# Kernel optimization log

Hardware: AMD Instinct MI355X
Metric: run time of the kernel (lower is better)

## Reference

```python
import jax, jax.numpy as jnp
import numpy as np

B, T, C = 2, 1024, 1024
H = 16
HS = C // H          # head size = 64
ROT = HS // 2        # partial rotary dims = 32
CTX = 1024           # ctx_len (T <= CTX)
FFN_H = 3 * 1024     # GeGLU hidden = 3 * n_ffn
LN_EPS = 1e-5


def setup_inputs():
    key = jax.random.key(0)
    ks = jax.random.split(key, 20)
    s = 0.02
    f32 = jnp.float32
    p = {}
    p["x"] = jax.random.normal(ks[0], (B, T, C), f32)
    p["ln1_w"] = jnp.ones((C,), f32); p["ln1_b"] = jnp.zeros((C,), f32)
    p["ln2_w"] = jnp.ones((C,), f32); p["ln2_b"] = jnp.zeros((C,), f32)
    p["Wq"] = jax.random.normal(ks[1], (C, C), f32) * s; p["bq"] = jnp.zeros((C,), f32)
    p["Wk"] = jax.random.normal(ks[2], (C, C), f32) * s; p["bk"] = jnp.zeros((C,), f32)
    p["Wv"] = jax.random.normal(ks[3], (C, C), f32) * s; p["bv"] = jnp.zeros((C,), f32)
    p["Wo"] = jax.random.normal(ks[4], (C, C), f32) * s; p["bo"] = jnp.zeros((C,), f32)
    p["time_w"] = 1.0 + 0.01 * jax.random.normal(ks[5], (H, CTX), f32)
    p["time_alpha"] = 1.0 + 0.01 * jax.random.normal(ks[6], (H, 1, CTX), f32)
    p["time_beta"] = 1.0 + 0.01 * jax.random.normal(ks[7], (H, CTX, 1), f32)
    p["time_gamma"] = 1.0 + 0.01 * jax.random.normal(ks[8], (CTX, 1), f32)
    p["mix_w"] = jnp.eye(H, dtype=f32) + 0.02 * jax.random.normal(ks[9], (H, H), f32)
    p["Wkg"] = jax.random.normal(ks[10], (C, FFN_H), f32) * s; p["bkg"] = jnp.zeros((FFN_H,), f32)
    p["Wvg"] = jax.random.normal(ks[11], (C, FFN_H), f32) * s; p["bvg"] = jnp.zeros((FFN_H,), f32)
    p["Wwg"] = jax.random.normal(ks[12], (FFN_H, C), f32) * s; p["bwg"] = jnp.zeros((C,), f32)
    return p


def _ln(x, w, b):
    m = jnp.mean(x, axis=-1, keepdims=True)
    v = jnp.mean((x - m) ** 2, axis=-1, keepdims=True)
    return (x - m) * jax.lax.rsqrt(v + LN_EPS) * w + b


def _time_shift_half(x):
    # ZeroPad2d((0,0,1,-1)) on the first C//2 channels: shift down by one step in time
    c = x.shape[-1]
    shifted = jnp.pad(x[:, :-1, : c // 2], ((0, 0), (1, 0), (0, 0)))
    return jnp.concatenate([shifted, x[:, :, c // 2 :]], axis=-1)


def _decay_w(time_w, time_alpha, time_beta):
    # Toeplitz trick: [H, CTX] -> circulant [H, CTX, CTX] of relative-time weights
    TT = CTX
    w = jnp.pad(time_w, ((0, 0), (0, TT)))                 # [H, 2TT]
    w = jnp.tile(w, (1, TT))[:, :-TT]                      # [H, 2TT*TT - TT]
    w = w.reshape(-1, TT, 2 * TT - 1)[:, :, TT - 1 :]      # [H, TT, TT]
    return w[:, :T, :T] * time_alpha[:, :, :T] * time_beta[:, :T, :]


def _rotate_half(x):
    x1, x2 = x[..., : x.shape[-1] // 2], x[..., x.shape[-1] // 2 :]
    return jnp.concatenate([-x2, x1], axis=-1)


def _apply_rotary(q, k):
    # q, k: [B, H, T, ROT]
    inv_freq = 1.0 / (10000.0 ** (jnp.arange(0, ROT, 2, dtype=jnp.float32) / ROT))
    t = jnp.arange(T, dtype=jnp.float32)
    freqs = t[:, None] * inv_freq[None, :]                 # [T, ROT//2]
    emb = jnp.concatenate([freqs, freqs], axis=-1)         # [T, ROT]
    cos, sin = jnp.cos(emb), jnp.sin(emb)
    q = q * cos + _rotate_half(q) * sin
    k = k * cos + _rotate_half(k) * sin
    return q, k


def _mha_pro(x, Wq, bq, Wk, bk, Wv, bv, Wo, bo,
             time_w, time_alpha, time_beta, time_gamma, mix_w):
    w = _decay_w(time_w, time_alpha, time_beta)            # [H, T, T]
    xs = _time_shift_half(x)
    q = (xs @ Wq + bq).reshape(B, T, H, HS).transpose(0, 2, 1, 3)
    k = (xs @ Wk + bk).reshape(B, T, H, HS).transpose(0, 2, 1, 3)
    v = (xs @ Wv + bv).reshape(B, T, H, HS).transpose(0, 2, 1, 3)
    qr, qp = q[..., :ROT], q[..., ROT:]
    kr, kp = k[..., :ROT], k[..., ROT:]
    qr, kr = _apply_rotary(qr, kr)
    q = jnp.concatenate([qr, qp], axis=-1)
    k = jnp.concatenate([kr, kp], axis=-1)
    att = jnp.einsum('bhqd,bhkd->bhqk', q, k) * (1.0 / np.sqrt(HS))
    causal = jnp.tril(jnp.ones((T, T), dtype=bool))
    att = jnp.where(causal, att, -jnp.inf)
    att = jax.nn.softmax(att, axis=-1)
    att = att * w                                          # learned time-decay reweighting
    att = jnp.einsum('oi,biqk->boqk', mix_w, att)          # 1x1 conv head mixing
    y = jnp.einsum('bhqk,bhkd->bhqd', att, v)
    y = y.transpose(0, 2, 1, 3).reshape(B, T, C)
    return (y @ Wo + bo) * time_gamma[:T, :]


def _geglu(x, Wkg, bkg, Wvg, bvg, Wwg, bwg):
    kk = x @ Wkg + bkg
    vv = x @ Wvg + bvg
    return (jax.nn.gelu(kk, approximate=False) * vv) @ Wwg + bwg


def _block(x, ln1_w, ln1_b, ln2_w, ln2_b, Wq, bq, Wk, bk, Wv, bv, Wo, bo,
           time_w, time_alpha, time_beta, time_gamma, mix_w,
           Wkg, bkg, Wvg, bvg, Wwg, bwg):
    x = x + _mha_pro(_ln(x, ln1_w, ln1_b), Wq, bq, Wk, bk, Wv, bv, Wo, bo,
                     time_w, time_alpha, time_beta, time_gamma, mix_w)
    x = x + _geglu(_ln(x, ln2_w, ln2_b), Wkg, bkg, Wvg, bvg, Wwg, bwg)
    return x


def reference(x, ln1_w, ln1_b, ln2_w, ln2_b, Wq, bq, Wk, bk, Wv, bv, Wo, bo,
              time_w, time_alpha, time_beta, time_gamma, mix_w,
              Wkg, bkg, Wvg, bvg, Wwg, bwg):
    return _block(x, ln1_w, ln1_b, ln2_w, ln2_b, Wq, bq, Wk, bk, Wv, bv, Wo, bo,
                  time_w, time_alpha, time_beta, time_gamma, mix_w,
                  Wkg, bkg, Wvg, bvg, Wwg, bwg)
```

## Files before the change

### kernel.cpp

```cpp
#include <hip/hip_runtime.h>
#include <cstdint>
#include <cstddef>
#include <cstdio>

#define B_   2
#define T_   1024
#define C_   1024
#define H_   16
#define HS_  64
#define FFN_ 3072

typedef __bf16   bf16x8 __attribute__((ext_vector_type(8)));
typedef float    f32x4  __attribute__((ext_vector_type(4)));
typedef float    f32x16 __attribute__((ext_vector_type(16)));
typedef uint16_t u16x8  __attribute__((ext_vector_type(8)));

__device__ __forceinline__ uint16_t f2bf(float f){
  uint32_t u = __float_as_uint(f);
  u += 0x7FFFu + ((u >> 16) & 1u);
  return (uint16_t)(u >> 16);
}
__device__ __forceinline__ float bf2f(uint16_t h){
  return __uint_as_float(((uint32_t)h) << 16);
}
__device__ __forceinline__ bf16x8 ldb8(const uint16_t* p){
  return __builtin_bit_cast(bf16x8, *reinterpret_cast<const u16x8*>(p));
}
__device__ __forceinline__ f32x4 mfma16(bf16x8 a, bf16x8 b, f32x4 c){
  return __builtin_amdgcn_mfma_f32_16x16x32_bf16(a, b, c, 0, 0, 0);
}

typedef __attribute__((address_space(1))) const uint32_t* gas_t;
typedef __attribute__((address_space(3))) uint32_t* las_t;
__device__ __forceinline__ void gl_lds16(const uint16_t* g, uint16_t* l){
  __builtin_amdgcn_global_load_lds((gas_t)g, (las_t)l, 16, 0, 0);
}

__global__ __launch_bounds__(256) void k_prep(
    const float* __restrict__ Wq, const float* __restrict__ Wk,
    const float* __restrict__ Wv, const float* __restrict__ Wo,
    const float* __restrict__ Wkg, const float* __restrict__ Wvg,
    const float* __restrict__ Wwg,
    const float* __restrict__ bq, const float* __restrict__ bk,
    const float* __restrict__ bv, const float* __restrict__ bkg,
    const float* __restrict__ bvg,
    const float* __restrict__ x, const float* __restrict__ ln1w,
    const float* __restrict__ ln1b,
    uint16_t* __restrict__ WqT, uint16_t* __restrict__ WkT,
    uint16_t* __restrict__ WvT, uint16_t* __restrict__ WoT,
    uint16_t* __restrict__ WkgT, uint16_t* __restrict__ WvgT,
    uint16_t* __restrict__ WwgT, float* __restrict__ bcat,
    uint16_t* __restrict__ xs)
{
  __shared__ float tile[32][33];
  __shared__ float red[8];
  const int id = blockIdx.x;
  const int tid = threadIdx.x;

  if (id < 13312){
    const float* in; uint16_t* outp; int R, Cc, bx, by;
    if (id < 4096){
      int w = id >> 10, r = id & 1023;
      in   = (w==0)?Wq:(w==1)?Wk:(w==2)?Wv:Wo;
      outp = (w==0)?WqT:(w==1)?WkT:(w==2)?WvT:WoT;
      R = 1024; Cc = 1024; bx = r & 31; by = r >> 5;
    } else if (id < 10240){
      int r = id - 4096; int w = r / 3072; r -= w*3072;
      in = w ? Wvg : Wkg; outp = w ? WvgT : WkgT;
      R = 1024; Cc = 3072; bx = r % 96; by = r / 96;
    } else {
      int r = id - 10240;
      in = Wwg; outp = WwgT; R = 3072; Cc = 1024;
      bx = r & 31; by = r >> 5;
    }
    int c0 = bx*32, r0 = by*32;
    int tx = tid & 31, ty = tid >> 5;
    #pragma unroll
    for (int i=0;i<4;i++) tile[ty+i*8][tx] = in[(size_t)(r0+ty+i*8)*Cc + c0+tx];
    __syncthreads();
    #pragma unroll
    for (int i=0;i<4;i++) outp[(size_t)(c0+ty+i*8)*R + r0+tx] = f2bf(tile[tx][ty+i*8]);
    return;
  }
  if (id < 13348){
    int i = (id - 13312)*256 + tid;
    float v;
    if      (i < 1024) v = bq[i];
    else if (i < 2048) v = bk[i-1024];
    else if (i < 3072) v = bv[i-2048];
    else if (i < 6144) v = bkg[i-3072];
    else               v = bvg[i-6144];
    bcat[i] = v;
    return;
  }
  {
    int row = id - 13348;
    int t = row & (T_-1);
    const float* xr = x + (size_t)row*C_;
    float4 v = reinterpret_cast<const float4*>(xr)[tid];
    float s  = v.x+v.y+v.z+v.w;
    float s2 = v.x*v.x+v.y*v.y+v.z*v.z+v.w*v.w;
    #pragma unroll
    for (int o=1;o<64;o<<=1){ s += __shfl_xor(s,o); s2 += __shfl_xor(s2,o); }
    int lane = tid & 63, wv = tid >> 6;
    if (lane == 0){ red[wv] = s; red[4+wv] = s2; }
    __syncthreads();
    s  = red[0]+red[1]+red[2]+red[3];
    s2 = red[4]+red[5]+red[6]+red[7];
    float mean = s * (1.f/1024.f);
    float var  = s2 * (1.f/1024.f) - mean*mean;
    float rs   = rsqrtf(var + 1e-5f);
    float vals[4] = {v.x, v.y, v.z, v.w};
    #pragma unroll
    for (int j=0;j<4;j++){
      int cc = tid*4 + j;
      float o_ = (vals[j]-mean)*rs*ln1w[cc] + ln1b[cc];
      uint16_t ob = f2bf(o_);
      if (cc < 512){
        if (t < T_-1) xs[(size_t)(row+1)*C_ + cc] = ob;
        if (t == 0)   xs[(size_t)row*C_ + cc] = 0;
      } else {
        xs[(size_t)row*C_ + cc] = ob;
      }
    }
  }
}

template<int SHIFT>
__global__ __launch_bounds__(256) void k_ln(const float* __restrict__ in,
                                            const float* __restrict__ w,
                                            const float* __restrict__ bia,
                                            uint16_t* __restrict__ out){
  int row = blockIdx.x;
  int t = row & (T_-1);
  const float* xr = in + (size_t)row*C_;
  float4 v = reinterpret_cast<const float4*>(xr)[threadIdx.x];
  float s  = v.x+v.y+v.z+v.w;
  float s2 = v.x*v.x+v.y*v.y+v.z*v.z+v.w*v.w;
  #pragma unroll
  for (int o=1;o<64;o<<=1){ s += __shfl_xor(s,o); s2 += __shfl_xor(s2,o); }
  __shared__ float red[8];
  int lane = threadIdx.x & 63, wid = threadIdx.x >> 6;
  if (lane == 0){ red[wid] = s; red[4+wid] = s2; }
  __syncthreads();
  s  = red[0]+red[1]+red[2]+red[3];
  s2 = red[4]+red[5]+red[6]+red[7];
  float mean = s * (1.f/1024.f);
  float var  = s2 * (1.f/1024.f) - mean*mean;
  float rs   = rsqrtf(var + 1e-5f);
  float vals[4] = {v.x, v.y, v.z, v.w};
  #pragma unroll
  for (int j=0;j<4;j++){
    int cc = threadIdx.x*4 + j;
    float o_ = (vals[j]-mean)*rs*w[cc] + bia[cc];
    uint16_t ob = f2bf(o_);
    if (SHIFT){
      if (cc < 512){
        if (t < T_-1) out[(size_t)(row+1)*C_ + cc] = ob;
        if (t == 0)   out[(size_t)row*C_ + cc] = 0;
      } else {
        out[(size_t)row*C_ + cc] = ob;
      }
    } else {
      out[(size_t)row*C_ + cc] = ob;
    }
  }
}

enum { EPI_QKV=0, EPI_WO=2, EPI_BF16=3, EPI_FFN2=4 };

template<int EPI, int BN>
__global__ __launch_bounds__(256) void k_gemm2(
    const uint16_t* __restrict__ A, const uint16_t* __restrict__ Bt,
    const float* __restrict__ bias, void* __restrict__ outp,
    int M, int N, int K,
    const float* __restrict__ aux0, const float* __restrict__ aux1)
{
  __shared__ uint16_t As[128*32];
  __shared__ uint16_t Bs[BN*32];
  const int m0 = blockIdx.y*128, n0 = blockIdx.x*BN;
  const int tid = threadIdx.x;
  const int lane = tid & 63, wid = tid >> 6;
  const int wy = wid >> 1, wx = wid & 1;
  const int l16 = lane & 15, lr = lane >> 4;
  const int WN = BN/2;
  const int NW = BN/32;
  const f32x4 z = {0.f,0.f,0.f,0.f};
  f32x4 acc[4][NW];
  #pragma unroll
  for (int m=0;m<4;m++)
    #pragma unroll
    for (int n=0;n<NW;n++) acc[m][n] = z;
  const int srow = tid >> 2, scol = (tid & 3)*8;
  for (int k0 = 0; k0 < K; k0 += 32){
    gl_lds16(A + (size_t)(m0 + srow)*K      + k0 + scol, As + tid*8);
    gl_lds16(A + (size_t)(m0 + 64 + srow)*K + k0 + scol, As + 2048 + tid*8);
    gl_lds16(Bt + (size_t)(n0 + srow)*K     + k0 + scol, Bs + tid*8);
    if constexpr (BN == 128)
      gl_lds16(Bt + (size_t)(n0 + 64 + srow)*K + k0 + scol, Bs + 2048 + tid*8);
    __syncthreads();
    bf16x8 af[4], bfr[NW];
    #pragma unroll
    for (int m=0;m<4;m++) af[m] = ldb8(As + (wy*64 + m*16 + l16)*32 + lr*8);
    #pragma unroll
    for (int n=0;n<NW;n++) bfr[n] = ldb8(Bs + (wx*WN + n*16 + l16)*32 + lr*8);
    #pragma unroll
    for (int m=0;m<4;m++)
      #pragma unroll
      for (int n=0;n<NW;n++) acc[m][n] = mfma16(af[m], bfr[n], acc[m][n]);
    __syncthreads();
  }
  if constexpr (EPI == EPI_QKV){
    const float linvf = exp2f(-(float)l16 * 0.83048202f);
    #pragma unroll
    for (int m=0;m<4;m++){
      #pragma unroll
      for (int r=0;r<4;r++){
        int row = m0 + wy*64 + m*16 + lr*4 + r;
        int bb = row >> 10, t = row & 1023;
        int col0 = n0 + wx*32 + l16;
        float v0 = acc[m][0][r] + bias[col0];
        float v1 = acc[m][1][r] + bias[col0+16];
        int kind = col0 >> 10, hcol = col0 & 1023;
        int h = hcol >> 6, d0 = hcol & 63;
        if (kind < 2 && wx == 0){
          float sn, cs;
          __sincosf((float)t * linvf, &sn, &cs);
          float r0 = v0*cs - v1*sn;
          float r1 = v1*cs + v0*sn;
          v0 = r0; v1 = r1;
        }
        uint16_t* dst = (uint16_t*)outp + (size_t)kind*2097152;
        if (kind < 2){
          size_t basei = (((size_t)bb*16 + h)*1024 + t)*64;
          dst[basei + d0]      = f2bf(v0);
          dst[basei + d0 + 16] = f2bf(v1);
        } else {
          size_t basei = ((size_t)bb*16 + h)*65536;
          dst[basei + (size_t)d0*1024 + t]      = f2bf(v0);
          dst[basei + (size_t)(d0+16)*1024 + t] = f2bf(v1);
        }
      }
    }
  } else {
    #pragma unroll
    for (int m=0;m<4;m++){
      #pragma unroll
      for (int n=0;n<NW;n++){
        int col = n0 + wx*WN + n*16 + l16;
        float bc_ = bias ? bias[col] : 0.f;
        #pragma unroll
        for (int r=0;r<4;r++){
          int row = m0 + wy*64 + m*16 + lr*4 + r;
          float v = acc[m][n][r] + bc_;
          if constexpr (EPI == EPI_WO){
            int t = row & (T_-1);
            ((float*)outp)[(size_t)row*N + col] = aux1[(size_t)row*N + col] + v*aux0[t];
          } else if constexpr (EPI == EPI_BF16){
            ((uint16_t*)outp)[(size_t)row*N + col] = f2bf(v);
          } else {
            ((float*)outp)[(size_t)row*N + col] = aux0[(size_t)row*N + col] + v;
          }
        }
      }
    }
  }
}

__global__ __launch_bounds__(256) void k_stats(const uint16_t* __restrict__ q,
                                               const uint16_t* __restrict__ kmat,
                                               float* __restrict__ sm, float* __restrict__ sl){
  int bh = blockIdx.x, qb = blockIdx.y;
  int lane = threadIdx.x & 63, wid = threadIdx.x >> 6;
  int l16 = lane & 15, lr = lane >> 4;
  int r0 = qb*64 + wid*16;
  const uint16_t* qh = q    + (size_t)bh*T_*HS_;
  const uint16_t* kh = kmat + (size_t)bh*T_*HS_;
  int kq = lr*8;
  bf16x8 a0 = ldb8(qh + (size_t)(r0 + l16)*HS_ + kq);
  bf16x8 a1 = ldb8(qh + (size_t)(r0 + l16)*HS_ + kq + 32);
  float m_[4], l_[4]; int rows[4];
  #pragma unroll
  for (int r=0;r<4;r++){ m_[r] = -1e30f; l_[r] = 0.f; rows[r] = r0 + lr*4 + r; }
  int ktmax = (r0 + 15) >> 4;
  for (int kt = 0; kt <= ktmax; kt++){
    bf16x8 b0 = ldb8(kh + (size_t)(kt*16 + l16)*HS_ + kq);
    bf16x8 b1 = ldb8(kh + (size_t)(kt*16 + l16)*HS_ + kq + 32);
    f32x4 s = {0.f,0.f,0.f,0.f};
    s = mfma16(a0, b0, s);
    s = mfma16(a1, b1, s);
    int kcol = kt*16 + l16;
    #pragma unroll
    for (int r=0;r<4;r++){
      float sv = (kcol <= rows[r]) ? s[r]*0.125f : -3.0e38f;
      float mn = fmaxf(m_[r], sv);
      l_[r] = l_[r]*__expf(m_[r] - mn) + __expf(sv - mn);
      m_[r] = mn;
    }
  }
  #pragma unroll
  for (int o=1;o<16;o<<=1){
    #pragma unroll
    for (int r=0;r<4;r++){
      float mo = __shfl_xor(m_[r], o);
      float lo = __shfl_xor(l_[r], o);
      float mn = fmaxf(m_[r], mo);
      l_[r] = l_[r]*__expf(m_[r] - mn) + lo*__expf(mo - mn);
      m_[r] = mn;
    }
  }
  if (l16 == 0){
    #pragma unroll
    for (int r=0;r<4;r++){
      sm[(size_t)bh*T_ + rows[r]] = m_[r];
      sl[(size_t)bh*T_ + rows[r]] = l_[r];
    }
  }
}

__global__ __launch_bounds__(512, 2) void k_attn(
    const uint16_t* __restrict__ q, const uint16_t* __restrict__ kmat,
    const uint16_t* __restrict__ vT,
    const float* __restrict__ sm, const float* __restrict__ sl,
    const float* __restrict__ tw, const float* __restrict__ alpha,
    const float* __restrict__ beta, const float* __restrict__ mixw,
    uint16_t* __restrict__ py)
{
  int qt = blockIdx.x, kc = blockIdx.y, b = blockIdx.z;
  if (8*kc > qt) return;
  const int q0 = qt*16, ck0 = kc*128;
  const int lc = min(127, q0 + 15 - ck0);
  const int nt = (lc >> 5) + 1;

  __shared__ uint32_t U32[2*4096];
  __shared__ uint16_t Cm[2*8320];
  __shared__ uint16_t TWL[16*160];

  const int tid = threadIdx.x;
  const int lane = tid & 63;
  const int wid = __builtin_amdgcn_readfirstlane(tid >> 6);
  const int l16 = lane & 15, lr = lane >> 4;
  const int l32 = lane & 31, g32 = lane >> 5;

  const int base = 1008 - q0 + ck0;
  for (int i = tid; i < 16*144; i += 512){
    int h = i / 144, t = i - h*144;
    int gi = base + t;
    TWL[h*160 + t] = (gi <= 1023) ? f2bf(tw[h*1024 + gi]) : (uint16_t)0;
  }

  float SM[2][4], BSL[2][4];
  bf16x8 qa[2][2];
  #pragma unroll
  for (int h2=0; h2<2; ++h2){
    int h = 2*wid + h2, bh = b*16 + h;
    float4 s4 = *reinterpret_cast<const float4*>(sm   + (size_t)bh*1024 + q0 + lr*4);
    float4 l4 = *reinterpret_cast<const float4*>(sl   + (size_t)bh*1024 + q0 + lr*4);
    float4 b4 = *reinterpret_cast<const float4*>(beta + (size_t)h*1024  + q0 + lr*4);
    SM[h2][0]=s4.x; SM[h2][1]=s4.y; SM[h2][2]=s4.z; SM[h2][3]=s4.w;
    BSL[h2][0]=b4.x/l4.x; BSL[h2][1]=b4.y/l4.y; BSL[h2][2]=b4.z/l4.z; BSL[h2][3]=b4.w/l4.w;
    #pragma unroll
    for (int kk=0;kk<2;kk++)
      qa[h2][kk] = ldb8(q + ((size_t)bh*1024 + q0 + l16)*64 + kk*32 + lr*8);
  }
  bf16x8 mwf;
  {
    u16x8 t8;
    #pragma unroll
    for (int j=0;j<8;j++){
      float v = (l32 < 16) ? mixw[l32*16 + g32*8 + j] : 0.f;
      t8[j] = f2bf(v);
    }
    mwf = __builtin_bit_cast(bf16x8, t8);
  }

  const f32x4 z = {0.f,0.f,0.f,0.f};
  f32x4 acc[2][4];
  #pragma unroll
  for (int oo=0;oo<2;oo++) for (int n=0;n<4;n++) acc[oo][n] = z;

  __syncthreads();

  for (int tp = 0; tp < nt; tp += 2){
    const int ntile = (nt - tp >= 2) ? 2 : 1;
    #pragma unroll
    for (int half = 0; half < 2; ++half){
      if (half >= ntile) break;
      const int t = tp + half;
      const int k0 = ck0 + t*32;
      float al0[2], al1[2];
      #pragma unroll
      for (int n=0;n<2;n++){
        int kg = k0 + n*16 + l16;
        al0[n] = alpha[(2*wid+0)*1024 + kg];
        al1[n] = alpha[(2*wid+1)*1024 + kg];
      }
      f32x4 s[2][2];
      s[0][0]=z; s[0][1]=z; s[1][0]=z; s[1][1]=z;
      #pragma unroll
      for (int h2=0;h2<2;h2++){
        const uint16_t* kh = kmat + ((size_t)(b*16 + 2*wid + h2)*1024 + k0)*64;
        #pragma unroll
        for (int kk=0;kk<2;kk++){
          bf16x8 kb0 = ldb8(kh + (size_t)(l16)*64      + kk*32 + lr*8);
          bf16x8 kb1 = ldb8(kh + (size_t)(16 + l16)*64 + kk*32 + lr*8);
          s[h2][0] = mfma16(qa[h2][kk], kb0, s[h2][0]);
          s[h2][1] = mfma16(qa[h2][kk], kb1, s[h2][1]);
        }
      }
      uint32_t* Ub = U32 + half*4096;
      #pragma unroll
      for (int n=0;n<2;n++){
        int kloc = n*16 + l16;
        int kg = k0 + kloc;
        #pragma unroll
        for (int r=0;r<4;r++){
          int qloc = lr*4 + r;
          bool ok = (kg <= q0 + qloc);
          int twi = 15 - qloc + (kg - ck0);
          float u0 = 0.f, u1 = 0.f;
          if (ok){
            u0 = __expf(s[0][n][r]*0.125f - SM[0][r]) * BSL[0][r] * al0[n] * bf2f(TWL[(2*wid+0)*160 + twi]);
            u1 = __expf(s[1][n][r]*0.125f - SM[1][r]) * BSL[1][r] * al1[n] * bf2f(TWL[(2*wid+1)*160 + twi]);
          }
          uint32_t pk = (uint32_t)f2bf(u0) | ((uint32_t)f2bf(u1) << 16);
          Ub[wid*512 + qloc*32 + ((kloc + 8*(qloc>>2)) & 31)] = pk;
        }
      }
    }
    __syncthreads();
    #pragma unroll
    for (int half = 0; half < 2; ++half){
      if (half >= ntile) break;
      const uint32_t* Ub = U32 + half*4096;
      uint16_t* Cb = Cm + half*8320;
      #pragma unroll
      for (int cc=0; cc<2; ++cc){
        int qrow = wid*2 + cc;
        int pbase = qrow*32;
        int swz = (l32 + 8*(qrow>>2)) & 31;
        u16x8 a8;
        uint32_t* a32 = reinterpret_cast<uint32_t*>(&a8);
        #pragma unroll
        for (int j=0;j<4;j++)
          a32[j] = Ub[(4*g32 + j)*512 + pbase + swz];
        bf16x8 a = __builtin_bit_cast(bf16x8, a8);
        f32x16 zz{};
        __builtin_amdgcn_s_setprio(1);
        f32x16 dd = __builtin_amdgcn_mfma_f32_32x32x16_bf16(a, mwf, zz, 0, 0, 0);
        __builtin_amdgcn_s_setprio(0);
        if (l32 < 16){
          int o = l32;
          #pragma unroll
          for (int rg=0; rg<4; ++rg){
            int p0 = pbase + rg*8 + g32*4;
            uint32_t w0 = (uint32_t)f2bf(dd[4*rg+0]) | ((uint32_t)f2bf(dd[4*rg+1]) << 16);
            uint32_t w1 = (uint32_t)f2bf(dd[4*rg+2]) | ((uint32_t)f2bf(dd[4*rg+3]) << 16);
            uint2 pk2; pk2.x = w0; pk2.y = w1;
            *reinterpret_cast<uint2*>(Cb + (size_t)o*520 + p0) = pk2;
          }
        }
      }
    }
    __syncthreads();
    #pragma unroll
    for (int half = 0; half < 2; ++half){
      if (half >= ntile) break;
      const int k0 = ck0 + (tp + half)*32;
      const uint16_t* Cb = Cm + half*8320;
      #pragma unroll
      for (int oo=0;oo<2;oo++){
        int o = 2*wid + oo;
        bf16x8 cf = ldb8(Cb + (size_t)o*520 + l16*32 + lr*8);
        const uint16_t* vh = vT + (size_t)(b*16 + o)*65536;
        __builtin_amdgcn_s_setprio(1);
        #pragma unroll
        for (int n=0;n<4;n++){
          bf16x8 vf = ldb8(vh + (size_t)(n*16 + l16)*1024 + k0 + lr*8);
          acc[oo][n] = mfma16(cf, vf, acc[oo][n]);
        }
        __builtin_amdgcn_s_setprio(0);
      }
    }
  }

  uint16_t* po = py + (((size_t)(b*64 + qt))*8 + kc)*16384;
  #pragma unroll
  for (int oo=0;oo<2;oo++){
    int o = 2*wid + oo;
    #pragma unroll
    for (int n=0;n<4;n++)
      #pragma unroll
      for (int r=0;r<4;r++){
        int qloc = lr*4 + r;
        po[o*1024 + qloc*64 + n*16 + l16] = f2bf(acc[oo][n][r]);
      }
  }
}

__global__ void k_yred(const uint16_t* __restrict__ py, uint16_t* __restrict__ y){
  int idx = blockIdx.x*256 + threadIdx.x;
  int d8 = idx & 7, qq = (idx>>3)&15, o = (idx>>7)&15, qt = (idx>>11)&63, b = idx>>17;
  int nch = (qt>>3) + 1;
  const uint16_t* p0 = py + (((size_t)(b*64+qt))*8)*16384 + o*1024 + qq*64 + d8*8;
  float s[8] = {0,0,0,0,0,0,0,0};
  for (int kc=0; kc<nch; kc++){
    u16x8 v = *reinterpret_cast<const u16x8*>(p0 + (size_t)kc*16384);
    #pragma unroll
    for (int e=0;e<8;e++) s[e] += bf2f(v[e]);
  }
  int t = qt*16 + qq;
  u16x8 w;
  #pragma unroll
  for (int e=0;e<8;e++) w[e] = f2bf(s[e]);
  *reinterpret_cast<u16x8*>(y + ((size_t)(b*1024 + t))*1024 + o*64 + d8*8) = w;
}

__global__ void k_geglu(const uint16_t* __restrict__ ffu, uint16_t* __restrict__ g){
  int i = blockIdx.x*256 + threadIdx.x;
  int row = i / 384, j8 = i - row*384;
  const uint16_t* pa = ffu + (size_t)row*6144 + j8*8;
  u16x8 a = *reinterpret_cast<const u16x8*>(pa);
  u16x8 b = *reinterpret_cast<const u16x8*>(pa + 3072);
  u16x8 o;
  #pragma unroll
  for (int e=0;e<8;e++){
    float xv = bf2f(a[e]);
    float gl = 0.5f*xv*(1.f + erff(xv*0.70710678118f));
    o[e] = f2bf(gl * bf2f(b[e]));
  }
  *reinterpret_cast<u16x8*>(g + (size_t)row*3072 + j8*8) = o;
}

extern "C" void kernel_launch(void* const* d_in, const int* in_sizes, int n_in,
                              void* d_out, int out_size, void* d_ws, size_t ws_size,
                              hipStream_t stream)
{
  const float* x      = (const float*)d_in[0];
  const float* ln1w   = (const float*)d_in[1];
  const float* ln1b   = (const float*)d_in[2];
  const float* ln2w   = (const float*)d_in[3];
  const float* ln2b   = (const float*)d_in[4];
  const float* Wq     = (const float*)d_in[5];
  const float* bq     = (const float*)d_in[6];
  const float* Wk     = (const float*)d_in[7];
  const float* bk     = (const float*)d_in[8];
  const float* Wv     = (const float*)d_in[9];
  const float* bv     = (const float*)d_in[10];
  const float* Wo     = (const float*)d_in[11];
  const float* bo     = (const float*)d_in[12];
  const float* tw     = (const float*)d_in[13];
  const float* talpha = (const float*)d_in[14];
  const float* tbeta  = (const float*)d_in[15];
  const float* tgamma = (const float*)d_in[16];
  const float* mixw   = (const float*)d_in[17];
  const float* Wkg    = (const float*)d_in[18];
  const float* bkg    = (const float*)d_in[19];
  const float* Wvg    = (const float*)d_in[20];
  const float* bvg    = (const float*)d_in[21];
  const float* Wwg    = (const float*)d_in[22];
  const float* bwg    = (const float*)d_in[23];

  char* ws = (char*)d_ws;
  size_t off = 0;
  auto alloc = [&](size_t bytes)->char*{
    char* p = ws + off; off += (bytes + 255) & ~(size_t)255; return p;
  };
  uint16_t* WqT  = (uint16_t*)alloc((size_t)C_*C_*2);
  uint16_t* WkT  = (uint16_t*)alloc((size_t)C_*C_*2);
  uint16_t* WvT  = (uint16_t*)alloc((size_t)C_*C_*2);
  uint16_t* WoT  = (uint16_t*)alloc((size_t)C_*C_*2);
  uint16_t* WkgT = (uint16_t*)alloc((size_t)FFN_*C_*2);
  uint16_t* WvgT = (uint16_t*)alloc((size_t)FFN_*C_*2);
  uint16_t* WwgT = (uint16_t*)alloc((size_t)C_*FFN_*2);
  uint16_t* xs   = (uint16_t*)alloc((size_t)B_*T_*C_*2);
  uint16_t* qbuf = (uint16_t*)alloc((size_t)B_*T_*C_*2);
  uint16_t* kbuf = (uint16_t*)alloc((size_t)B_*T_*C_*2);
  uint16_t* vT   = (uint16_t*)alloc((size_t)B_*T_*C_*2);
  float*    sm   = (float*)alloc((size_t)B_*H_*T_*4);
  float*    sl   = (float*)alloc((size_t)B_*H_*T_*4);
  uint16_t* ybuf = (uint16_t*)alloc((size_t)B_*T_*C_*2);
  float*    x1   = (float*)alloc((size_t)B_*T_*C_*4);
  float*    bcat = (float*)alloc((size_t)9216*4);
  char*     region = alloc((size_t)64*1024*1024);
  uint16_t* py  = (uint16_t*)region;
  uint16_t* ffu = (uint16_t*)region;
  uint16_t* gb  = (uint16_t*)(region + (size_t)2048*6144*2);

  if (off > ws_size){
    fprintf(stderr, "kernel_launch: ws too small (%zu needed, %zu given)\n", off, ws_size);
    return;
  }

  dim3 blk(256);
  k_prep<<<15396, blk, 0, stream>>>(Wq, Wk, Wv, Wo, Wkg, Wvg, Wwg,
                                    bq, bk, bv, bkg, bvg,
                                    x, ln1w, ln1b,
                                    WqT, WkT, WvT, WoT, WkgT, WvgT, WwgT,
                                    bcat, xs);

  k_gemm2<EPI_QKV,64><<<dim3(48,16), blk, 0, stream>>>(xs, WqT, bcat, qbuf, 2048, 3072, 1024, nullptr, nullptr);

  k_stats<<<dim3(B_*H_, T_/64), blk, 0, stream>>>(qbuf, kbuf, sm, sl);
  k_attn<<<dim3(64,8,B_), dim3(512), 0, stream>>>(qbuf, kbuf, vT, sm, sl,
                                                  tw, talpha, tbeta, mixw, py);
  k_yred<<<1024, blk, 0, stream>>>(py, ybuf);

  k_gemm2<EPI_WO,64><<<dim3(16,16), blk, 0, stream>>>(ybuf, WoT, bo, x1, 2048, 1024, 1024, tgamma, x);

  k_ln<0><<<B_*T_, blk, 0, stream>>>(x1, ln2w, ln2b, xs);

  k_gemm2<EPI_BF16,128><<<dim3(48,16), blk, 0, stream>>>(xs, WkgT, bcat+3072, ffu, 2048, 6144, 1024, nullptr, nullptr);
  k_geglu<<<3072, blk, 0, stream>>>(ffu, gb);
  k_gemm2<EPI_FFN2,64><<<dim3(16,16), blk, 0, stream>>>(gb, WwgT, bwg, d_out, 2048, 1024, 3072, x1, nullptr);
}
```

Measured before the change: 276.7 us.

## Fuse GeGLU into FFN1 GEMM epilogue and use persistent attention scheduling

The GeLU and gate product move into the first FFN GEMM epilogue. The Wkg/Wvg weights and biases are interleaved in 16-column groups, so each warp holds matching k and v accumulator fragments. This drops the 2048x6144 bf16 intermediate round-trip and the separate k_geglu launch. The attention kernel also becomes a persistent grid of 512 blocks pulling causal work items from an atomic counter, instead of launching 64x8x2 blocks where many exit immediately; this costs a memset plus an atomic and barrier per item.

```diff
diff --git a/kernel.cpp b/kernel.cpp
--- a/kernel.cpp
+++ b/kernel.cpp
@@ -48,8 +48,8 @@
     const float* __restrict__ ln1b,
     uint16_t* __restrict__ WqT, uint16_t* __restrict__ WkT,
     uint16_t* __restrict__ WvT, uint16_t* __restrict__ WoT,
-    uint16_t* __restrict__ WkgT, uint16_t* __restrict__ WvgT,
-    uint16_t* __restrict__ WwgT, float* __restrict__ bcat,
+    uint16_t* __restrict__ Wff, uint16_t* __restrict__ WwgT,
+    float* __restrict__ bcat, float* __restrict__ bcatFF,
     uint16_t* __restrict__ xs)
 {
   __shared__ float tile[32][33];
@@ -58,39 +58,57 @@
   const int tid = threadIdx.x;
 
   if (id < 13312){
-    const float* in; uint16_t* outp; int R, Cc, bx, by;
     if (id < 4096){
       int w = id >> 10, r = id & 1023;
-      in   = (w==0)?Wq:(w==1)?Wk:(w==2)?Wv:Wo;
-      outp = (w==0)?WqT:(w==1)?WkT:(w==2)?WvT:WoT;
-      R = 1024; Cc = 1024; bx = r & 31; by = r >> 5;
+      const float* in = (w==0)?Wq:(w==1)?Wk:(w==2)?Wv:Wo;
+      uint16_t* outp  = (w==0)?WqT:(w==1)?WkT:(w==2)?WvT:WoT;
+      int c0 = (r & 31)*32, r0 = (r >> 5)*32;
+      int tx = tid & 31, ty = tid >> 5;
+      #pragma unroll
+      for (int i=0;i<4;i++) tile[ty+i*8][tx] = in[(size_t)(r0+ty+i*8)*1024 + c0+tx];
+      __syncthreads();
+      #pragma unroll
+      for (int i=0;i<4;i++) outp[(size_t)(c0+ty+i*8)*1024 + r0+tx] = f2bf(tile[tx][ty+i*8]);
     } else if (id < 10240){
-      int r = id - 4096; int w = r / 3072; r -= w*3072;
-      in = w ? Wvg : Wkg; outp = w ? WvgT : WkgT;
-      R = 1024; Cc = 3072; bx = r % 96; by = r / 96;
+      int r = id - 4096; int s = r / 3072; r -= s*3072;
+      const float* in = s ? Wvg : Wkg;
+      int c0 = (r % 96)*32, r0 = (r / 96)*32;
+      int tx = tid & 31, ty = tid >> 5;
+      #pragma unroll
+      for (int i=0;i<4;i++) tile[ty+i*8][tx] = in[(size_t)(r0+ty+i*8)*3072 + c0+tx];
+      __syncthreads();
+      #pragma unroll
+      for (int i=0;i<4;i++){
+        int j = c0+ty+i*8;
+        int row = ((j>>4)<<5) + (s<<4) + (j&15);
+        Wff[(size_t)row*1024 + r0+tx] = f2bf(tile[tx][ty+i*8]);
+      }
     } else {
       int r = id - 10240;
-      in = Wwg; outp = WwgT; R = 3072; Cc = 1024;
-      bx = r & 31; by = r >> 5;
-    }
-    int c0 = bx*32, r0 = by*32;
-    int tx = tid & 31, ty = tid >> 5;
-    #pragma unroll
-    for (int i=0;i<4;i++) tile[ty+i*8][tx] = in[(size_t)(r0+ty+i*8)*Cc + c0+tx];
-    __syncthreads();
-    #pragma unroll
-    for (int i=0;i<4;i++) outp[(size_t)(c0+ty+i*8)*R + r0+tx] = f2bf(tile[tx][ty+i*8]);
+      int c0 = (r & 31)*32, r0 = (r >> 5)*32;
+      int tx = tid & 31, ty = tid >> 5;
+      #pragma unroll
+      for (int i=0;i<4;i++) tile[ty+i*8][tx] = Wwg[(size_t)(r0+ty+i*8)*1024 + c0+tx];
+      __syncthreads();
+      #pragma unroll
+      for (int i=0;i<4;i++) WwgT[(size_t)(c0+ty+i*8)*3072 + r0+tx] = f2bf(tile[tx][ty+i*8]);
+    }
     return;
   }
-  if (id < 13348){
+  if (id < 13324){
     int i = (id - 13312)*256 + tid;
     float v;
     if      (i < 1024) v = bq[i];
     else if (i < 2048) v = bk[i-1024];
-    else if (i < 3072) v = bv[i-2048];
-    else if (i < 6144) v = bkg[i-3072];
-    else               v = bvg[i-6144];
+    else               v = bv[i-2048];
     bcat[i] = v;
+    return;
+  }
+  if (id < 13348){
+    int i = (id - 13324)*256 + tid;
+    int s = (i >> 4) & 1;
+    int j = ((i >> 5) << 4) | (i & 15);
+    bcatFF[i] = s ? bvg[j] : bkg[j];
     return;
   }
   {
@@ -126,13 +144,11 @@
   }
 }
 
-template<int SHIFT>
 __global__ __launch_bounds__(256) void k_ln(const float* __restrict__ in,
                                             const float* __restrict__ w,
                                             const float* __restrict__ bia,
                                             uint16_t* __restrict__ out){
   int row = blockIdx.x;
-  int t = row & (T_-1);
   const float* xr = in + (size_t)row*C_;
   float4 v = reinterpret_cast<const float4*>(xr)[threadIdx.x];
   float s  = v.x+v.y+v.z+v.w;
@@ -152,22 +168,11 @@
   #pragma unroll
   for (int j=0;j<4;j++){
     int cc = threadIdx.x*4 + j;
-    float o_ = (vals[j]-mean)*rs*w[cc] + bia[cc];
-    uint16_t ob = f2bf(o_);
-    if (SHIFT){
-      if (cc < 512){
-        if (t < T_-1) out[(size_t)(row+1)*C_ + cc] = ob;
-        if (t == 0)   out[(size_t)row*C_ + cc] = 0;
-      } else {
-        out[(size_t)row*C_ + cc] = ob;
-      }
-    } else {
-      out[(size_t)row*C_ + cc] = ob;
-    }
-  }
-}
-
-enum { EPI_QKV=0, EPI_WO=2, EPI_BF16=3, EPI_FFN2=4 };
+    out[(size_t)row*C_ + cc] = f2bf((vals[j]-mean)*rs*w[cc] + bia[cc]);
+  }
+}
+
+enum { EPI_QKV=0, EPI_WO=2, EPI_GEGLU=3, EPI_FFN2=4 };
 
 template<int EPI, int BN>
 __global__ __launch_bounds__(256) void k_gemm2(
@@ -242,6 +247,23 @@
         }
       }
     }
+  } else if constexpr (EPI == EPI_GEGLU){
+    const int colb = n0 + wx*WN;
+    #pragma unroll
+    for (int m=0;m<4;m++){
+      #pragma unroll
+      for (int r=0;r<4;r++){
+        int row = m0 + wy*64 + m*16 + lr*4 + r;
+        #pragma unroll
+        for (int np=0;np<NW;np+=2){
+          float kk = acc[m][np][r]   + bias[colb + np*16 + l16];
+          float vv = acc[m][np+1][r] + bias[colb + (np+1)*16 + l16];
+          float gl = 0.5f*kk*(1.f + erff(kk*0.70710678118f));
+          int j = ((colb>>5) + (np>>1))*16 + l16;
+          ((uint16_t*)outp)[(size_t)row*3072 + j] = f2bf(gl*vv);
+        }
+      }
+    }
   } else {
     #pragma unroll
     for (int m=0;m<4;m++){
@@ -256,8 +278,6 @@
           if constexpr (EPI == EPI_WO){
             int t = row & (T_-1);
             ((float*)outp)[(size_t)row*N + col] = aux1[(size_t)row*N + col] + v*aux0[t];
-          } else if constexpr (EPI == EPI_BF16){
-            ((uint16_t*)outp)[(size_t)row*N + col] = f2bf(v);
           } else {
             ((float*)outp)[(size_t)row*N + col] = aux0[(size_t)row*N + col] + v;
           }
@@ -324,17 +344,12 @@
     const float* __restrict__ sm, const float* __restrict__ sl,
     const float* __restrict__ tw, const float* __restrict__ alpha,
     const float* __restrict__ beta, const float* __restrict__ mixw,
-    uint16_t* __restrict__ py)
+    uint16_t* __restrict__ py, int* __restrict__ counter)
 {
-  int qt = blockIdx.x, kc = blockIdx.y, b = blockIdx.z;
-  if (8*kc > qt) return;
-  const int q0 = qt*16, ck0 = kc*128;
-  const int lc = min(127, q0 + 15 - ck0);
-  const int nt = (lc >> 5) + 1;
-
   __shared__ uint32_t U32[2*4096];
   __shared__ uint16_t Cm[2*8320];
   __shared__ uint16_t TWL[16*160];
+  __shared__ int s_item;
 
   const int tid = threadIdx.x;
   const int lane = tid & 63;
@@ -342,27 +357,6 @@
   const int l16 = lane & 15, lr = lane >> 4;
   const int l32 = lane & 31, g32 = lane >> 5;
 
-  const int base = 1008 - q0 + ck0;
-  for (int i = tid; i < 16*144; i += 512){
-    int h = i / 144, t = i - h*144;
-    int gi = base + t;
-    TWL[h*160 + t] = (gi <= 1023) ? f2bf(tw[h*1024 + gi]) : (uint16_t)0;
-  }
-
-  float SM[2][4], BSL[2][4];
-  bf16x8 qa[2][2];
-  #pragma unroll
-  for (int h2=0; h2<2; ++h2){
-    int h = 2*wid + h2, bh = b*16 + h;
-    float4 s4 = *reinterpret_cast<const float4*>(sm   + (size_t)bh*1024 + q0 + lr*4);
-    float4 l4 = *reinterpret_cast<const float4*>(sl   + (size_t)bh*1024 + q0 + lr*4);
-    float4 b4 = *reinterpret_cast<const float4*>(beta + (size_t)h*1024  + q0 + lr*4);
-    SM[h2][0]=s4.x; SM[h2][1]=s4.y; SM[h2][2]=s4.z; SM[h2][3]=s4.w;
-    BSL[h2][0]=b4.x/l4.x; BSL[h2][1]=b4.y/l4.y; BSL[h2][2]=b4.z/l4.z; BSL[h2][3]=b4.w/l4.w;
-    #pragma unroll
-    for (int kk=0;kk<2;kk++)
-      qa[h2][kk] = ldb8(q + ((size_t)bh*1024 + q0 + l16)*64 + kk*32 + lr*8);
-  }
   bf16x8 mwf;
   {
     u16x8 t8;
@@ -373,128 +367,168 @@
     }
     mwf = __builtin_bit_cast(bf16x8, t8);
   }
-
   const f32x4 z = {0.f,0.f,0.f,0.f};
-  f32x4 acc[2][4];
-  #pragma unroll
-  for (int oo=0;oo<2;oo++) for (int n=0;n<4;n++) acc[oo][n] = z;
-
-  __syncthreads();
-
-  for (int tp = 0; tp < nt; tp += 2){
-    const int ntile = (nt - tp >= 2) ? 2 : 1;
-    #pragma unroll
-    for (int half = 0; half < 2; ++half){
-      if (half >= ntile) break;
-      const int t = tp + half;
-      const int k0 = ck0 + t*32;
-      float al0[2], al1[2];
-      #pragma unroll
-      for (int n=0;n<2;n++){
-        int kg = k0 + n*16 + l16;
-        al0[n] = alpha[(2*wid+0)*1024 + kg];
-        al1[n] = alpha[(2*wid+1)*1024 + kg];
-      }
-      f32x4 s[2][2];
-      s[0][0]=z; s[0][1]=z; s[1][0]=z; s[1][1]=z;
-      #pragma unroll
-      for (int h2=0;h2<2;h2++){
-        const uint16_t* kh = kmat + ((size_t)(b*16 + 2*wid + h2)*1024 + k0)*64;
-        #pragma unroll
-        for (int kk=0;kk<2;kk++){
-          bf16x8 kb0 = ldb8(kh + (size_t)(l16)*64      + kk*32 + lr*8);
-          bf16x8 kb1 = ldb8(kh + (size_t)(16 + l16)*64 + kk*32 + lr*8);
-          s[h2][0] = mfma16(qa[h2][kk], kb0, s[h2][0]);
-          s[h2][1] = mfma16(qa[h2][kk], kb1, s[h2][1]);
-        }
-      }
-      uint32_t* Ub = U32 + half*4096;
-      #pragma unroll
-      for (int n=0;n<2;n++){
-        int kloc = n*16 + l16;
-        int kg = k0 + kloc;
+
+  for (;;){
+    if (tid == 0) s_item = atomicAdd(counter, 1);
+    __syncthreads();
+    const int item = s_item;
+    if (item >= 576) break;
+
+    const int b = (item >= 288) ? 1 : 0;
+    int j = item - b*288;
+    int g = 0;
+    while (4*(g+1)*(g+2) <= j) g++;
+    int jj = j - 4*g*(g+1);
+    const int qt = 8*g + jj/(g+1);
+    const int kc = jj % (g+1);
+
+    const int q0 = qt*16, ck0 = kc*128;
+    const int lc = min(127, q0 + 15 - ck0);
+    const int nt = (lc >> 5) + 1;
+
+    const int base = 1008 - q0 + ck0;
+    for (int i = tid; i < 16*144; i += 512){
+      int h = i / 144, t = i - h*144;
+      int gi = base + t;
+      TWL[h*160 + t] = (gi <= 1023) ? f2bf(tw[h*1024 + gi]) : (uint16_t)0;
+    }
+    float SM[2][4], BSL[2][4];
+    bf16x8 qa[2][2];
+    #pragma unroll
+    for (int h2=0; h2<2; ++h2){
+      int h = 2*wid + h2, bh = b*16 + h;
+      float4 s4 = *reinterpret_cast<const float4*>(sm   + (size_t)bh*1024 + q0 + lr*4);
+      float4 l4 = *reinterpret_cast<const float4*>(sl   + (size_t)bh*1024 + q0 + lr*4);
+      float4 b4 = *reinterpret_cast<const float4*>(beta + (size_t)h*1024  + q0 + lr*4);
+      SM[h2][0]=s4.x; SM[h2][1]=s4.y; SM[h2][2]=s4.z; SM[h2][3]=s4.w;
+      BSL[h2][0]=b4.x/l4.x; BSL[h2][1]=b4.y/l4.y; BSL[h2][2]=b4.z/l4.z; BSL[h2][3]=b4.w/l4.w;
+      #pragma unroll
+      for (int kk=0;kk<2;kk++)
+        qa[h2][kk] = ldb8(q + ((size_t)bh*1024 + q0 + l16)*64 + kk*32 + lr*8);
+    }
+    f32x4 acc[2][4];
+    #pragma unroll
+    for (int oo=0;oo<2;oo++) for (int n=0;n<4;n++) acc[oo][n] = z;
+
+    __syncthreads();
+
+    for (int tp = 0; tp < nt; tp += 2){
+      const int ntile = (nt - tp >= 2) ? 2 : 1;
+      #pragma unroll
+      for (int half = 0; half < 2; ++half){
+        if (half >= ntile) break;
+        const int t = tp + half;
+        const int k0 = ck0 + t*32;
+        float al0[2], al1[2];
+        #pragma unroll
+        for (int n=0;n<2;n++){
+          int kg = k0 + n*16 + l16;
+          al0[n] = alpha[(2*wid+0)*1024 + kg];
+          al1[n] = alpha[(2*wid+1)*1024 + kg];
+        }
+        f32x4 s[2][2];
+        s[0][0]=z; s[0][1]=z; s[1][0]=z; s[1][1]=z;
+        #pragma unroll
+        for (int h2=0;h2<2;h2++){
+          const uint16_t* kh = kmat + ((size_t)(b*16 + 2*wid + h2)*1024 + k0)*64;
+          #pragma unroll
+          for (int kk=0;kk<2;kk++){
+            bf16x8 kb0 = ldb8(kh + (size_t)(l16)*64      + kk*32 + lr*8);
+            bf16x8 kb1 = ldb8(kh + (size_t)(16 + l16)*64 + kk*32 + lr*8);
+            s[h2][0] = mfma16(qa[h2][kk], kb0, s[h2][0]);
+            s[h2][1] = mfma16(qa[h2][kk], kb1, s[h2][1]);
+          }
+        }
+        uint32_t* Ub = U32 + half*4096;
+        #pragma unroll
+        for (int n=0;n<2;n++){
+          int kloc = n*16 + l16;
+          int kg = k0 + kloc;
+          #pragma unroll
+          for (int r=0;r<4;r++){
+            int qloc = lr*4 + r;
+            bool ok = (kg <= q0 + qloc);
+            int twi = 15 - qloc + (kg - ck0);
+            float u0 = 0.f, u1 = 0.f;
+            if (ok){
+              u0 = __expf(s[0][n][r]*0.125f - SM[0][r]) * BSL[0][r] * al0[n] * bf2f(TWL[(2*wid+0)*160 + twi]);
+              u1 = __expf(s[1][n][r]*0.125f - SM[1][r]) * BSL[1][r] * al1[n] * bf2f(TWL[(2*wid+1)*160 + twi]);
+            }
+            uint32_t pk = (uint32_t)f2bf(u0) | ((uint32_t)f2bf(u1) << 16);
+            Ub[wid*512 + qloc*32 + ((kloc + 8*(qloc>>2)) & 31)] = pk;
+          }
+        }
+      }
+      __syncthreads();
+      #pragma unroll
+      for (int half = 0; half < 2; ++half){
+        if (half >= ntile) break;
+        const uint32_t* Ub = U32 + half*4096;
+        uint16_t* Cb = Cm + half*8320;
+        #pragma unroll
+        for (int cc=0; cc<2; ++cc){
+          int qrow = wid*2 + cc;
+          int pbase = qrow*32;
+          int swz = (l32 + 8*(qrow>>2)) & 31;
+          u16x8 a8;
+          uint32_t* a32 = reinterpret_cast<uint32_t*>(&a8);
+          #pragma unroll
+          for (int jv=0;jv<4;jv++)
+            a32[jv] = Ub[(4*g32 + jv)*512 + pbase + swz];
+          bf16x8 a = __builtin_bit_cast(bf16x8, a8);
+          f32x16 zz{};
+          __builtin_amdgcn_s_setprio(1);
+          f32x16 dd = __builtin_amdgcn_mfma_f32_32x32x16_bf16(a, mwf, zz, 0, 0, 0);
+          __builtin_amdgcn_s_setprio(0);
+          if (l32 < 16){
+            int o = l32;
+            #pragma unroll
+            for (int rg=0; rg<4; ++rg){
+              int p0 = pbase + rg*8 + g32*4;
+              uint32_t w0 = (uint32_t)f2bf(dd[4*rg+0]) | ((uint32_t)f2bf(dd[4*rg+1]) << 16);
+              uint32_t w1 = (uint32_t)f2bf(dd[4*rg+2]) | ((uint32_t)f2bf(dd[4*rg+3]) << 16);
+              uint2 pk2; pk2.x = w0; pk2.y = w1;
+              *reinterpret_cast<uint2*>(Cb + (size_t)o*520 + p0) = pk2;
+            }
+          }
+        }
+      }
+      __syncthreads();
+      #pragma unroll
+      for (int half = 0; half < 2; ++half){
+        if (half >= ntile) break;
+        const int k0 = ck0 + (tp + half)*32;
+        const uint16_t* Cb = Cm + half*8320;
+        #pragma unroll
+        for (int oo=0;oo<2;oo++){
+          int o = 2*wid + oo;
+          bf16x8 cf = ldb8(Cb + (size_t)o*520 + l16*32 + lr*8);
+          const uint16_t* vh = vT + (size_t)(b*16 + o)*65536;
+          __builtin_amdgcn_s_setprio(1);
+          #pragma unroll
+          for (int n=0;n<4;n++){
+            bf16x8 vf = ldb8(vh + (size_t)(n*16 + l16)*1024 + k0 + lr*8);
+            acc[oo][n] = mfma16(cf, vf, acc[oo][n]);
+          }
+          __builtin_amdgcn_s_setprio(0);
+        }
+      }
+    }
+
+    uint16_t* po = py + (((size_t)(b*64 + qt))*8 + kc)*16384;
+    #pragma unroll
+    for (int oo=0;oo<2;oo++){
+      int o = 2*wid + oo;
+      #pragma unroll
+      for (int n=0;n<4;n++)
         #pragma unroll
         for (int r=0;r<4;r++){
           int qloc = lr*4 + r;
-          bool ok = (kg <= q0 + qloc);
-          int twi = 15 - qloc + (kg - ck0);
-          float u0 = 0.f, u1 = 0.f;
-          if (ok){
-            u0 = __expf(s[0][n][r]*0.125f - SM[0][r]) * BSL[0][r] * al0[n] * bf2f(TWL[(2*wid+0)*160 + twi]);
-            u1 = __expf(s[1][n][r]*0.125f - SM[1][r]) * BSL[1][r] * al1[n] * bf2f(TWL[(2*wid+1)*160 + twi]);
-          }
-          uint32_t pk = (uint32_t)f2bf(u0) | ((uint32_t)f2bf(u1) << 16);
-          Ub[wid*512 + qloc*32 + ((kloc + 8*(qloc>>2)) & 31)] = pk;
-        }
-      }
+          po[o*1024 + qloc*64 + n*16 + l16] = f2bf(acc[oo][n][r]);
+        }
     }
     __syncthreads();
-    #pragma unroll
-    for (int half = 0; half < 2; ++half){
-      if (half >= ntile) break;
-      const uint32_t* Ub = U32 + half*4096;
-      uint16_t* Cb = Cm + half*8320;
-      #pragma unroll
-      for (int cc=0; cc<2; ++cc){
-        int qrow = wid*2 + cc;
-        int pbase = qrow*32;
-        int swz = (l32 + 8*(qrow>>2)) & 31;
-        u16x8 a8;
-        uint32_t* a32 = reinterpret_cast<uint32_t*>(&a8);
-        #pragma unroll
-        for (int j=0;j<4;j++)
-          a32[j] = Ub[(4*g32 + j)*512 + pbase + swz];
-        bf16x8 a = __builtin_bit_cast(bf16x8, a8);
-        f32x16 zz{};
-        __builtin_amdgcn_s_setprio(1);
-        f32x16 dd = __builtin_amdgcn_mfma_f32_32x32x16_bf16(a, mwf, zz, 0, 0, 0);
-        __builtin_amdgcn_s_setprio(0);
-        if (l32 < 16){
-          int o = l32;
-          #pragma unroll
-          for (int rg=0; rg<4; ++rg){
-            int p0 = pbase + rg*8 + g32*4;
-            uint32_t w0 = (uint32_t)f2bf(dd[4*rg+0]) | ((uint32_t)f2bf(dd[4*rg+1]) << 16);
-            uint32_t w1 = (uint32_t)f2bf(dd[4*rg+2]) | ((uint32_t)f2bf(dd[4*rg+3]) << 16);
-            uint2 pk2; pk2.x = w0; pk2.y = w1;
-            *reinterpret_cast<uint2*>(Cb + (size_t)o*520 + p0) = pk2;
-          }
-        }
-      }
-    }
-    __syncthreads();
-    #pragma unroll
-    for (int half = 0; half < 2; ++half){
-      if (half >= ntile) break;
-      const int k0 = ck0 + (tp + half)*32;
-      const uint16_t* Cb = Cm + half*8320;
-      #pragma unroll
-      for (int oo=0;oo<2;oo++){
-        int o = 2*wid + oo;
-        bf16x8 cf = ldb8(Cb + (size_t)o*520 + l16*32 + lr*8);
-        const uint16_t* vh = vT + (size_t)(b*16 + o)*65536;
-        __builtin_amdgcn_s_setprio(1);
-        #pragma unroll
-        for (int n=0;n<4;n++){
-          bf16x8 vf = ldb8(vh + (size_t)(n*16 + l16)*1024 + k0 + lr*8);
-          acc[oo][n] = mfma16(cf, vf, acc[oo][n]);
-        }
-        __builtin_amdgcn_s_setprio(0);
-      }
-    }
-  }
-
-  uint16_t* po = py + (((size_t)(b*64 + qt))*8 + kc)*16384;
-  #pragma unroll
-  for (int oo=0;oo<2;oo++){
-    int o = 2*wid + oo;
-    #pragma unroll
-    for (int n=0;n<4;n++)
-      #pragma unroll
-      for (int r=0;r<4;r++){
-        int qloc = lr*4 + r;
-        po[o*1024 + qloc*64 + n*16 + l16] = f2bf(acc[oo][n][r]);
-      }
   }
 }
 
@@ -514,22 +548,6 @@
   #pragma unroll
   for (int e=0;e<8;e++) w[e] = f2bf(s[e]);
   *reinterpret_cast<u16x8*>(y + ((size_t)(b*1024 + t))*1024 + o*64 + d8*8) = w;
-}
-
-__global__ void k_geglu(const uint16_t* __restrict__ ffu, uint16_t* __restrict__ g){
-  int i = blockIdx.x*256 + threadIdx.x;
-  int row = i / 384, j8 = i - row*384;
-  const uint16_t* pa = ffu + (size_t)row*6144 + j8*8;
-  u16x8 a = *reinterpret_cast<const u16x8*>(pa);
-  u16x8 b = *reinterpret_cast<const u16x8*>(pa + 3072);
-  u16x8 o;
-  #pragma unroll
-  for (int e=0;e<8;e++){
-    float xv = bf2f(a[e]);
-    float gl = 0.5f*xv*(1.f + erff(xv*0.70710678118f));
-    o[e] = f2bf(gl * bf2f(b[e]));
-  }
-  *reinterpret_cast<u16x8*>(g + (size_t)row*3072 + j8*8) = o;
 }
 
 extern "C" void kernel_launch(void* const* d_in, const int* in_sizes, int n_in,
@@ -566,12 +584,12 @@
   auto alloc = [&](size_t bytes)->char*{
     char* p = ws + off; off += (bytes + 255) & ~(size_t)255; return p;
   };
+  int*      counter = (int*)alloc(256);
   uint16_t* WqT  = (uint16_t*)alloc((size_t)C_*C_*2);
   uint16_t* WkT  = (uint16_t*)alloc((size_t)C_*C_*2);
   uint16_t* WvT  = (uint16_t*)alloc((size_t)C_*C_*2);
   uint16_t* WoT  = (uint16_t*)alloc((size_t)C_*C_*2);
-  uint16_t* WkgT = (uint16_t*)alloc((size_t)FFN_*C_*2);
-  uint16_t* WvgT = (uint16_t*)alloc((size_t)FFN_*C_*2);
+  uint16_t* Wff  = (uint16_t*)alloc((size_t)2*FFN_*C_*2);
   uint16_t* WwgT = (uint16_t*)alloc((size_t)C_*FFN_*2);
   uint16_t* xs   = (uint16_t*)alloc((size_t)B_*T_*C_*2);
   uint16_t* qbuf = (uint16_t*)alloc((size_t)B_*T_*C_*2);
@@ -581,36 +599,37 @@
   float*    sl   = (float*)alloc((size_t)B_*H_*T_*4);
   uint16_t* ybuf = (uint16_t*)alloc((size_t)B_*T_*C_*2);
   float*    x1   = (float*)alloc((size_t)B_*T_*C_*4);
-  float*    bcat = (float*)alloc((size_t)9216*4);
-  char*     region = alloc((size_t)64*1024*1024);
+  float*    bcat   = (float*)alloc((size_t)3072*4);
+  float*    bcatFF = (float*)alloc((size_t)6144*4);
+  char*     region = alloc((size_t)33*1024*1024);
   uint16_t* py  = (uint16_t*)region;
-  uint16_t* ffu = (uint16_t*)region;
-  uint16_t* gb  = (uint16_t*)(region + (size_t)2048*6144*2);
+  uint16_t* gb  = (uint16_t*)region;
 
   if (off > ws_size){
     fprintf(stderr, "kernel_launch: ws too small (%zu needed, %zu given)\n", off, ws_size);
     return;
   }
+
+  hipMemsetAsync(counter, 0, 4, stream);
 
   dim3 blk(256);
   k_prep<<<15396, blk, 0, stream>>>(Wq, Wk, Wv, Wo, Wkg, Wvg, Wwg,
                                     bq, bk, bv, bkg, bvg,
                                     x, ln1w, ln1b,
-                                    WqT, WkT, WvT, WoT, WkgT, WvgT, WwgT,
-                                    bcat, xs);
+                                    WqT, WkT, WvT, WoT, Wff, WwgT,
+                                    bcat, bcatFF, xs);
 
   k_gemm2<EPI_QKV,64><<<dim3(48,16), blk, 0, stream>>>(xs, WqT, bcat, qbuf, 2048, 3072, 1024, nullptr, nullptr);
 
   k_stats<<<dim3(B_*H_, T_/64), blk, 0, stream>>>(qbuf, kbuf, sm, sl);
-  k_attn<<<dim3(64,8,B_), dim3(512), 0, stream>>>(qbuf, kbuf, vT, sm, sl,
-                                                  tw, talpha, tbeta, mixw, py);
+  k_attn<<<dim3(512), dim3(512), 0, stream>>>(qbuf, kbuf, vT, sm, sl,
+                                              tw, talpha, tbeta, mixw, py, counter);
   k_yred<<<1024, blk, 0, stream>>>(py, ybuf);
 
   k_gemm2<EPI_WO,64><<<dim3(16,16), blk, 0, stream>>>(ybuf, WoT, bo, x1, 2048, 1024, 1024, tgamma, x);
 
-  k_ln<0><<<B_*T_, blk, 0, stream>>>(x1, ln2w, ln2b, xs);
-
-  k_gemm2<EPI_BF16,128><<<dim3(48,16), blk, 0, stream>>>(xs, WkgT, bcat+3072, ffu, 2048, 6144, 1024, nullptr, nullptr);
-  k_geglu<<<3072, blk, 0, stream>>>(ffu, gb);
+  k_ln<<<B_*T_, blk, 0, stream>>>(x1, ln2w, ln2b, xs);
+
+  k_gemm2<EPI_GEGLU,128><<<dim3(48,16), blk, 0, stream>>>(xs, Wff, bcatFF, gb, 2048, 6144, 1024, nullptr, nullptr);
   k_gemm2<EPI_FFN2,64><<<dim3(16,16), blk, 0, stream>>>(gb, WwgT, bwg, d_out, 2048, 1024, 3072, x1, nullptr);
 }
```

Result: faster. 270.4 us (-2.3%).
